# Performance work log

Measured on AMD Instinct MI355X. Metric: run time of the kernel, lower is better.

The kernel has to match this reference:

```python
import jax, jax.numpy as jnp
import numpy as np

VOCAB = 30000  # opts.numofingr
EPS = 1e-12


def setup_inputs() -> dict:
    key = jax.random.key(0)
    ks = jax.random.split(key, 8)
    B, L = 4096, 20
    ingrs = jax.random.randint(ks[0], (B, L), 0, VOCAB, dtype=jnp.int32)
    lengths = jax.random.randint(ks[1], (B,), 0, 21, dtype=jnp.int32)
    # MLP params: Linear(VOCAB,512) -> ReLU -> Linear(512,1024) -> ReLU -> Linear(1024,2047)
    # Stored so that one-hot @ W1 == W1[ingr]; i.e. W1 has shape [VOCAB, 512].
    W1 = jax.random.normal(ks[2], (VOCAB, 512), dtype=jnp.float32) * (1.0 / np.sqrt(VOCAB))
    b1 = jax.random.normal(ks[3], (512,), dtype=jnp.float32) * 0.01
    W2 = jax.random.normal(ks[4], (512, 1024), dtype=jnp.float32) * (1.0 / np.sqrt(512))
    b2 = jax.random.normal(ks[5], (1024,), dtype=jnp.float32) * 0.01
    W3 = jax.random.normal(ks[6], (1024, 2047), dtype=jnp.float32) * (1.0 / np.sqrt(1024))
    b3 = jax.random.normal(ks[7], (2047,), dtype=jnp.float32) * 0.01
    return {"ingrs": ingrs, "lengths": lengths,
            "W1": W1, "b1": b1, "W2": W2, "b2": b2, "W3": W3, "b3": b3}


def reference(ingrs, lengths, W1, b1, W2, b2, W3, b3):
    # One-hot x MLP first layer == embedding row gather: [B, L, 512]
    h1 = jax.nn.relu(W1[ingrs] + b1)
    h2 = jax.nn.relu(jnp.einsum('blh,hk->blk', h1, W2) + b2)   # [B, L, 1024]
    emb = jnp.einsum('blk,ko->blo', h2, W3) + b3               # [B, L, 2047]
    # L2-normalize each ingredient embedding (torch norm(p=2, dim=1) on [1,2047])
    nrm = jnp.sqrt(jnp.sum(emb * emb, axis=-1, keepdims=True))
    emb = emb / jnp.maximum(nrm, EPS)
    # Masked sum over valid ingredients (ingr_ln truncation in the source)
    L = ingrs.shape[1]
    mask = (jnp.arange(L)[None, :] < lengths[:, None]).astype(emb.dtype)  # [B, L]
    return jnp.einsum('blo,bl->bo', emb, mask)                 # [B, 2047]
```

## Files before the change

kernel.cpp:

```cpp
#include <hip/hip_runtime.h>

#define VOCAB 30000
#define MPAD  30080
#define G_MT  120

typedef __attribute__((ext_vector_type(8))) short bf16x8;
typedef __attribute__((ext_vector_type(4))) float f32x4;

__device__ __forceinline__ unsigned short f2bf(float f) {
    unsigned int u = __builtin_bit_cast(unsigned int, f);
    u += 0x7fffu + ((u >> 16) & 1u);
    return (unsigned short)(u >> 16);
}
__device__ __forceinline__ float bf2f(unsigned int h) {
    unsigned int u = h << 16;
    return __builtin_bit_cast(float, u);
}

__device__ __forceinline__ void async16(const void* g, void* l) {
    __builtin_amdgcn_global_load_lds(
        (__attribute__((address_space(1))) void*)g,
        (__attribute__((address_space(3))) void*)l, 16, 0, 0);
}

__global__ void k_mark(const int* __restrict__ ingrs, const int* __restrict__ lengths,
                       int* __restrict__ flags, int* __restrict__ cnt)
{
    const int i = blockIdx.x * 256 + threadIdx.x;
    if (i == 0) *cnt = 0;
    if (i >= 4096 * 20) return;
    const int b = i / 20;
    const int l = i - b * 20;
    if (l < lengths[b]) flags[ingrs[i]] = 1;
}

__global__ void k_assign(const int* __restrict__ flags, int* __restrict__ remap,
                         int* __restrict__ cnt)
{
    const int i = blockIdx.x * 256 + threadIdx.x;
    if (i < VOCAB && flags[i] == 1) remap[i] = atomicAdd(cnt, 1);
}

__device__ __forceinline__ void transpose_body(
    const float* __restrict__ in, unsigned short* __restrict__ out,
    int K, int Nin, int n0, int k0, int tid, float (*t)[65])
{
#pragma unroll
    for (int p = 0; p < 16; ++p) {
        const int lin = p * 256 + tid;
        const int kk = lin >> 6, nn = lin & 63;
        const int n = n0 + nn;
        t[kk][nn] = (n < Nin) ? in[(size_t)(k0 + kk) * Nin + n] : 0.f;
    }
    __syncthreads();
#pragma unroll
    for (int p = 0; p < 16; ++p) {
        const int lin = p * 256 + tid;
        const int nn = lin >> 6, kk = lin & 63;
        out[(size_t)(n0 + nn) * K + k0 + kk] = f2bf(t[kk][nn]);
    }
}

#define MF(a, b, c) __builtin_amdgcn_mfma_f32_16x16x32_bf16(a, b, c, 0, 0, 0)

#define G_U(AB, H, B_, T) do {                                                 \
        const unsigned short* _s = ((AB) ? gB : gA)                            \
            + (size_t)((H) * 128) * K + (size_t)(T) * 64;                      \
        unsigned short* _d = &lds[(AB) * 32768 + (B_) * 16384                  \
            + ((H) * 128) * 64 + dst0];                                        \
        async16(_s, _d);                                                       \
        async16(_s + (size_t)8 * K, _d + 8 * 64);                              \
    } while (0)

#define LDA(I, S) (*(const bf16x8*)&lds[cb + ((wr * 128 + (I) * 16 + ml) * 64) + ((((S) * 4 + q) ^ m7) * 8)])
#define LDB(J, S) (*(const bf16x8*)&lds[32768 + cb + ((wc * 64 + (J) * 16 + ml) * 64) + ((((S) * 4 + q) ^ m7) * 8)])

#define G_MFMA16(AI0, BF)                                                      \
        _Pragma("unroll")                                                      \
        for (int i = 0; i < 4; ++i)                                            \
        _Pragma("unroll")                                                      \
        for (int j = 0; j < 4; ++j)                                            \
            acc[(AI0) + i][j] = MF(afr[i], BF[j], acc[(AI0) + i][j]);

#define G_BAR()  __builtin_amdgcn_s_barrier()
#define G_LGKM() do { asm volatile("s_waitcnt lgkmcnt(0)" ::: "memory");       \
                      __builtin_amdgcn_sched_barrier(0); } while (0)

__device__ __forceinline__ void gemm256_body(
    unsigned short* lds,
    const unsigned short* __restrict__ A, const unsigned short* __restrict__ BT,
    const float* __restrict__ bias, int bias_n, unsigned short* __restrict__ C,
    int K, int NK, int N, int relu, int mc, int id, int nt_shift)
{
    const int w  = id >> 3;
    const int n_tile = w & ((1 << nt_shift) - 1);
    const int m_tile = (id & 7) + ((w >> nt_shift) << 3);
    const int m0 = m_tile * 256;
    if (m0 >= mc) return;
    const int n0 = n_tile * 256;

    const int tid  = threadIdx.x;
    const int lane = tid & 63;
    const int w0   = tid >> 6;
    const int wr   = w0 >> 2;
    const int wc   = w0 & 3;
    const int q    = lane >> 4;
    const int ml   = lane & 15;
    const int m7   = ml & 7;

    f32x4 acc[8][4];
    const f32x4 zero = {0.f, 0.f, 0.f, 0.f};
#pragma unroll
    for (int i = 0; i < 8; ++i)
#pragma unroll
        for (int j = 0; j < 4; ++j) acc[i][j] = zero;

    const int rg = lane >> 3;
    const int kc = (lane & 7) ^ rg;
    const unsigned short* gA = A  + (size_t)(m0 + w0 * 16 + rg) * K + kc * 8;
    const unsigned short* gB = BT + (size_t)(n0 + w0 * 16 + rg) * K + kc * 8;
    const int dst0 = (w0 * 16) * 64 + lane * 8;

    G_U(0, 0, 0, 0); G_U(0, 1, 0, 0); G_U(1, 0, 0, 0); G_U(1, 1, 0, 0);
    G_U(0, 0, 1, 1); G_U(1, 0, 1, 1);
    asm volatile("s_waitcnt vmcnt(4)" ::: "memory");
    G_BAR();

    for (int t = 0; t < NK; ++t) {
        const int cb  = (t & 1) * 16384;
        const int nxt = (t & 1) ^ 1;
        bf16x8 afr[4], bS0[4], bS1[4];

#pragma unroll
        for (int j = 0; j < 4; ++j) bS0[j] = LDB(j, 0);
#pragma unroll
        for (int i = 0; i < 4; ++i) afr[i] = LDA(i, 0);
        if (t + 1 < NK) G_U(0, 1, nxt, t + 1);
        G_BAR(); G_LGKM();
        __builtin_amdgcn_s_setprio(1);
        G_MFMA16(0, bS0)
        __builtin_amdgcn_s_setprio(0);
        G_BAR();

#pragma unroll
        for (int i = 0; i < 4; ++i) afr[i] = LDA(4 + i, 0);
        if (t + 1 < NK) G_U(1, 1, nxt, t + 1);
        G_BAR(); G_LGKM();
        __builtin_amdgcn_s_setprio(1);
        G_MFMA16(4, bS0)
        __builtin_amdgcn_s_setprio(0);
        G_BAR();

#pragma unroll
        for (int j = 0; j < 4; ++j) bS1[j] = LDB(j, 1);
#pragma unroll
        for (int i = 0; i < 4; ++i) afr[i] = LDA(i, 1);
        G_BAR(); G_LGKM();
        __builtin_amdgcn_s_setprio(1);
        G_MFMA16(0, bS1)
        __builtin_amdgcn_s_setprio(0);
        G_BAR();

#pragma unroll
        for (int i = 0; i < 4; ++i) afr[i] = LDA(4 + i, 1);
        if (t + 2 < NK) { G_U(0, 0, t & 1, t + 2); G_U(1, 0, t & 1, t + 2); }
        G_BAR(); G_LGKM();
        __builtin_amdgcn_s_setprio(1);
        G_MFMA16(4, bS1)
        __builtin_amdgcn_s_setprio(0);
        if (t + 2 < NK) asm volatile("s_waitcnt vmcnt(4)" ::: "memory");
        else            asm volatile("s_waitcnt vmcnt(0)" ::: "memory");
        G_BAR();
    }

    float bv[4];
#pragma unroll
    for (int j = 0; j < 4; ++j) {
        const int col = n0 + wc * 64 + j * 16 + ml;
        bv[j] = (col < bias_n) ? bias[col] : 0.f;
    }
    for (int h = 0; h < 2; ++h) {
        if (wr == h) {
#pragma unroll
            for (int i = 0; i < 8; ++i)
#pragma unroll
                for (int j = 0; j < 4; ++j)
#pragma unroll
                    for (int r = 0; r < 4; ++r) {
                        float v = acc[i][j][r] + bv[j];
                        if (relu) v = fmaxf(v, 0.f);
                        lds[(i * 16 + q * 4 + r) * 280 + wc * 64 + j * 16 + ml] = f2bf(v);
                    }
        }
        __syncthreads();
#pragma unroll
        for (int p = 0; p < 8; ++p) {
            const int row  = p * 16 + (tid >> 5);
            const int c8   = (tid & 31) * 8;
            const int grow = m0 + h * 128 + row;
            if (grow < MPAD) {
                *(uint4*)&C[(size_t)grow * N + n0 + c8] =
                    *(const uint4*)&lds[row * 280 + c8];
            }
        }
        __syncthreads();
    }
}

__global__ __launch_bounds__(256)
void k_prep(const float* __restrict__ W1, const float* __restrict__ b1,
            const int* __restrict__ flags, const int* __restrict__ remap,
            unsigned short* __restrict__ A1,
            const float* __restrict__ W2, unsigned short* __restrict__ W2T,
            const float* __restrict__ W3, unsigned short* __restrict__ W3T,
            const int* __restrict__ ingrs, const int* __restrict__ lengths,
            int* __restrict__ slots)
{
    __shared__ float t[64][65];
    const int bid = blockIdx.x;
    const int tid = threadIdx.x;

    if (bid < 15000) {
        const int id = bid * 2 + (tid >> 7);
        if (flags[id] != 1) return;
        const int row = remap[id];
        const int k4  = (tid & 127) * 4;
        const float4 w  = *(const float4*)(W1 + (size_t)id * 512 + k4);
        const float4 bb = *(const float4*)(b1 + k4);
        unsigned short o[4];
        o[0] = f2bf(fmaxf(w.x + bb.x, 0.f));
        o[1] = f2bf(fmaxf(w.y + bb.y, 0.f));
        o[2] = f2bf(fmaxf(w.z + bb.z, 0.f));
        o[3] = f2bf(fmaxf(w.w + bb.w, 0.f));
        *(uint2*)(A1 + (size_t)row * 512 + k4) = *(const uint2*)o;
    } else if (bid < 15128) {
        const int local = bid - 15000;
        transpose_body(W2, W2T, 512, 1024, (local & 15) * 64, (local >> 4) * 64, tid, t);
    } else if (bid < 15640) {
        const int local = bid - 15128;
        transpose_body(W3, W3T, 1024, 2047, (local & 31) * 64, (local >> 5) * 64, tid, t);
    } else {
        const int i = (bid - 15640) * 256 + tid;
        if (i < 4096 * 20) {
            const int b = i / 20;
            const int l = i - b * 20;
            if (l < lengths[b]) slots[i] = remap[ingrs[i]];
        }
    }
}

__global__ __launch_bounds__(512, 2)
void k_gemm1(const unsigned short* __restrict__ A1, const unsigned short* __restrict__ W2T,
             const float* __restrict__ b2, unsigned short* __restrict__ H2,
             const int* __restrict__ cnt)
{
    __shared__ __align__(16) unsigned short lds[65536];
    const int mc = (*cnt + 255) & ~255;
    gemm256_body(lds, A1, W2T, b2, 1024, H2, 512, 8, 1024, 1, mc, blockIdx.x, 2);
}

__global__ __launch_bounds__(512, 2)
void k_gemm2(const unsigned short* __restrict__ H2, const unsigned short* __restrict__ W3T,
             const float* __restrict__ b3, unsigned short* __restrict__ Table,
             const int* __restrict__ cnt)
{
    __shared__ __align__(16) unsigned short lds[65536];
    const int mc = (*cnt + 255) & ~255;
    gemm256_body(lds, H2, W3T, b3, 2047, Table, 1024, 16, 2048, 0, mc, blockIdx.x, 3);
}

__global__ __launch_bounds__(64)
void k_gather(const int* __restrict__ lengths, const int* __restrict__ slots,
              const unsigned short* __restrict__ Table, float* __restrict__ out)
{
    const int b    = blockIdx.x;
    const int lane = threadIdx.x;

    float acc[32];
#pragma unroll
    for (int j = 0; j < 32; ++j) acc[j] = 0.f;

    const int len = lengths[b];
    if (len > 0) {
        uint4 u0[4], u1[4], u2[4];
        {
            const uint4* rp = (const uint4*)(Table + (size_t)slots[b * 20] * 2048);
#pragma unroll
            for (int c = 0; c < 4; ++c) u0[c] = rp[c * 64 + lane];
        }
        if (len > 1) {
            const uint4* rp = (const uint4*)(Table + (size_t)slots[b * 20 + 1] * 2048);
#pragma unroll
            for (int c = 0; c < 4; ++c) u1[c] = rp[c * 64 + lane];
        }
        if (len > 2) {
            const uint4* rp = (const uint4*)(Table + (size_t)slots[b * 20 + 2] * 2048);
#pragma unroll
            for (int c = 0; c < 4; ++c) u2[c] = rp[c * 64 + lane];
        }
        for (int l = 0; l < len; ++l) {
            uint4 cu[4];
#pragma unroll
            for (int c = 0; c < 4; ++c) { cu[c] = u0[c]; u0[c] = u1[c]; u1[c] = u2[c]; }
            if (l + 3 < len) {
                const uint4* rp = (const uint4*)(Table + (size_t)slots[b * 20 + l + 3] * 2048);
#pragma unroll
                for (int c = 0; c < 4; ++c) u2[c] = rp[c * 64 + lane];
            }
            float v[32];
#pragma unroll
            for (int c = 0; c < 4; ++c) {
                v[c*8+0] = bf2f(cu[c].x & 0xffffu); v[c*8+1] = bf2f(cu[c].x >> 16);
                v[c*8+2] = bf2f(cu[c].y & 0xffffu); v[c*8+3] = bf2f(cu[c].y >> 16);
                v[c*8+4] = bf2f(cu[c].z & 0xffffu); v[c*8+5] = bf2f(cu[c].z >> 16);
                v[c*8+6] = bf2f(cu[c].w & 0xffffu); v[c*8+7] = bf2f(cu[c].w >> 16);
            }
            float s = 0.f;
#pragma unroll
            for (int j = 0; j < 32; ++j) s += v[j] * v[j];
#pragma unroll
            for (int off = 1; off < 64; off <<= 1) s += __shfl_xor(s, off, 64);
            const float invn = 1.0f / fmaxf(sqrtf(s), 1e-12f);
#pragma unroll
            for (int j = 0; j < 32; ++j) acc[j] += v[j] * invn;
        }
    }

    const size_t base = (size_t)b * 2047;
#pragma unroll
    for (int c = 0; c < 4; ++c) {
        const int col = (c * 64 + lane) * 8;
        if (c < 3 || lane != 63) {
            *(float4*)&out[base + col]     = *(const float4*)&acc[c * 8];
            *(float4*)&out[base + col + 4] = *(const float4*)&acc[c * 8 + 4];
        } else {
#pragma unroll
            for (int j = 0; j < 7; ++j) out[base + col + j] = acc[c * 8 + j];
        }
    }
}


extern "C" void kernel_launch(void* const* d_in, const int* in_sizes, int n_in,
                              void* d_out, int out_size, void* d_ws, size_t ws_size,
                              hipStream_t stream)
{
    const int*   ingrs   = (const int*)d_in[0];
    const int*   lengths = (const int*)d_in[1];
    const float* W1 = (const float*)d_in[2];
    const float* b1 = (const float*)d_in[3];
    const float* W2 = (const float*)d_in[4];
    const float* b2 = (const float*)d_in[5];
    const float* W3 = (const float*)d_in[6];
    const float* b3 = (const float*)d_in[7];
    float* out = (float*)d_out;

    char* ws = (char*)d_ws;
    unsigned short* A1    = (unsigned short*)(ws);
    unsigned short* H2    = (unsigned short*)(ws + 30801920);
    unsigned short* Table = (unsigned short*)(ws + 92405760);
    unsigned short* W2T   = (unsigned short*)(ws + 215613440);
    unsigned short* W3T   = (unsigned short*)(ws + 216662016);
    int*            flags = (int*)(ws + 220856320);
    int*            remap = (int*)(ws + 220976320);
    int*            cnt   = (int*)(ws + 221096320);
    int*            slots = (int*)(ws + 221216448);

    k_mark  <<<(4096 * 20 + 255) / 256, 256, 0, stream>>>(ingrs, lengths, flags, cnt);
    k_assign<<<(VOCAB + 255) / 256, 256, 0, stream>>>(flags, remap, cnt);
    k_prep<<<15960, 256, 0, stream>>>(W1, b1, flags, remap, A1, W2, W2T,
                                      W3, W3T, ingrs, lengths, slots);
    k_gemm1<<<G_MT * 4, 512, 0, stream>>>(A1, W2T, b2, H2, cnt);
    k_gemm2<<<G_MT * 8, 512, 0, stream>>>(H2, W3T, b3, Table, cnt);

    k_gather<<<4096, 64, 0, stream>>>(lengths, slots, Table, out);
}
```

Before: 309.5 us.

## Fuse the two MLP GEMMs into one kernel with per-row readiness flags

Merges the layer-2 and layer-3 GEMM kernels into a single launch. Every block first pulls layer-2 tiles from a global atomic work counter and bumps a per-256-row ready counter after finishing each tile. Each block then computes its assigned layer-3 tile once that row block's four layer-2 tiles are marked ready. This removes the kernel boundary and lets the tail of the first GEMM overlap with the start of the second. In exchange it adds spin-waiting, atomics and an acquire/release dependency, and it drops the min-blocks launch bound, which may change register allocation.

```diff
diff --git a/kernel.cpp b/kernel.cpp
--- a/kernel.cpp
+++ b/kernel.cpp
@@ -35,9 +35,14 @@
 }
 
 __global__ void k_assign(const int* __restrict__ flags, int* __restrict__ remap,
-                         int* __restrict__ cnt)
+                         int* __restrict__ cnt, int* __restrict__ ready,
+                         int* __restrict__ g1next)
 {
     const int i = blockIdx.x * 256 + threadIdx.x;
+    if (blockIdx.x == 0) {
+        if (threadIdx.x < 128) ready[threadIdx.x] = 0;
+        else if (threadIdx.x == 128) *g1next = 0;
+    }
     if (i < VOCAB && flags[i] == 1) remap[i] = atomicAdd(cnt, 1);
 }
 
@@ -86,19 +91,12 @@
 #define G_LGKM() do { asm volatile("s_waitcnt lgkmcnt(0)" ::: "memory");       \
                       __builtin_amdgcn_sched_barrier(0); } while (0)
 
-__device__ __forceinline__ void gemm256_body(
+__device__ __forceinline__ void gemm_tile(
     unsigned short* lds,
     const unsigned short* __restrict__ A, const unsigned short* __restrict__ BT,
     const float* __restrict__ bias, int bias_n, unsigned short* __restrict__ C,
-    int K, int NK, int N, int relu, int mc, int id, int nt_shift)
-{
-    const int w  = id >> 3;
-    const int n_tile = w & ((1 << nt_shift) - 1);
-    const int m_tile = (id & 7) + ((w >> nt_shift) << 3);
-    const int m0 = m_tile * 256;
-    if (m0 >= mc) return;
-    const int n0 = n_tile * 256;
-
+    int K, int NK, int N, int relu, int m0, int n0)
+{
     const int tid  = threadIdx.x;
     const int lane = tid & 63;
     const int w0   = tid >> 6;
@@ -249,24 +247,47 @@
     }
 }
 
-__global__ __launch_bounds__(512, 2)
-void k_gemm1(const unsigned short* __restrict__ A1, const unsigned short* __restrict__ W2T,
-             const float* __restrict__ b2, unsigned short* __restrict__ H2,
-             const int* __restrict__ cnt)
+__global__ __launch_bounds__(512)
+void k_gemm12(const unsigned short* __restrict__ A1, const unsigned short* __restrict__ W2T,
+              const float* __restrict__ b2, unsigned short* __restrict__ H2,
+              const unsigned short* __restrict__ W3T, const float* __restrict__ b3,
+              unsigned short* __restrict__ Table, const int* __restrict__ cnt,
+              int* __restrict__ ready, int* __restrict__ g1next)
 {
     __shared__ __align__(16) unsigned short lds[65536];
+    __shared__ int sh_t;
+
     const int mc = (*cnt + 255) & ~255;
-    gemm256_body(lds, A1, W2T, b2, 1024, H2, 512, 8, 1024, 1, mc, blockIdx.x, 2);
-}
-
-__global__ __launch_bounds__(512, 2)
-void k_gemm2(const unsigned short* __restrict__ H2, const unsigned short* __restrict__ W3T,
-             const float* __restrict__ b3, unsigned short* __restrict__ Table,
-             const int* __restrict__ cnt)
-{
-    __shared__ __align__(16) unsigned short lds[65536];
-    const int mc = (*cnt + 255) & ~255;
-    gemm256_body(lds, H2, W3T, b3, 2047, Table, 1024, 16, 2048, 0, mc, blockIdx.x, 3);
+    const int nm = mc >> 8;
+    const int tid = threadIdx.x;
+
+    for (;;) {
+        if (tid == 0)
+            sh_t = __hip_atomic_fetch_add(g1next, 1, __ATOMIC_RELAXED,
+                                          __HIP_MEMORY_SCOPE_AGENT);
+        __syncthreads();
+        const int t = sh_t;
+        __syncthreads();
+        if (t >= nm * 4) break;
+        const int m = t >> 2, n = t & 3;
+        gemm_tile(lds, A1, W2T, b2, 1024, H2, 512, 8, 1024, 1, m * 256, n * 256);
+        __syncthreads();
+        if (tid == 0)
+            __hip_atomic_fetch_add(&ready[m], 1, __ATOMIC_RELEASE,
+                                   __HIP_MEMORY_SCOPE_AGENT);
+        __syncthreads();
+    }
+
+    const int bid = blockIdx.x;
+    const int m2 = bid >> 3, n2 = bid & 7;
+    if (m2 >= nm) return;
+    if (tid == 0) {
+        while (__hip_atomic_load(&ready[m2], __ATOMIC_ACQUIRE,
+                                 __HIP_MEMORY_SCOPE_AGENT) < 4)
+            __builtin_amdgcn_s_sleep(8);
+    }
+    __syncthreads();
+    gemm_tile(lds, H2, W3T, b3, 2047, Table, 1024, 16, 2048, 0, m2 * 256, n2 * 256);
 }
 
 __global__ __launch_bounds__(64)
@@ -364,14 +385,15 @@
     int*            flags = (int*)(ws + 220856320);
     int*            remap = (int*)(ws + 220976320);
     int*            cnt   = (int*)(ws + 221096320);
+    int*            ready = (int*)(ws + 221096448);
+    int*            g1next= (int*)(ws + 221096960);
     int*            slots = (int*)(ws + 221216448);
 
     k_mark  <<<(4096 * 20 + 255) / 256, 256, 0, stream>>>(ingrs, lengths, flags, cnt);
-    k_assign<<<(VOCAB + 255) / 256, 256, 0, stream>>>(flags, remap, cnt);
+    k_assign<<<(VOCAB + 255) / 256, 256, 0, stream>>>(flags, remap, cnt, ready, g1next);
     k_prep<<<15960, 256, 0, stream>>>(W1, b1, flags, remap, A1, W2, W2T,
                                       W3, W3T, ingrs, lengths, slots);
-    k_gemm1<<<G_MT * 4, 512, 0, stream>>>(A1, W2T, b2, H2, cnt);
-    k_gemm2<<<G_MT * 8, 512, 0, stream>>>(H2, W3T, b3, Table, cnt);
-
+    k_gemm12<<<G_MT * 8, 512, 0, stream>>>(A1, W2T, b2, H2, W3T, b3, Table,
+                                           cnt, ready, g1next);
     k_gather<<<4096, 64, 0, stream>>>(lengths, slots, Table, out);
 }
```

Result: slower. 348.3 us (+12.5%).
